# Kernel tuning notes

Hardware: AMD Instinct MI355X
Metric: run time of the kernel (lower is better)

Reference implementation:

```python
import jax, jax.numpy as jnp
import numpy as np

NUM_HEADS = 12
DIM = 768
HEAD_DIM = DIM // NUM_HEADS
NUM_BUCKETS = 32
MAX_DISTANCE = 128
ELEV_SCALE = 1000.0


def _bucket_positions(relative_position):
    # Faithful port of RelativePositionBias2D._bucket_positions (torch .long() truncates;
    # values passed through the large branch are non-negative so astype(int32) matches).
    nb = NUM_BUCKETS // 2  # 16
    n = -relative_position
    ret = (n < 0).astype(jnp.int32) * nb
    n = jnp.abs(n)
    max_exact = nb // 2  # 8
    is_small = n < max_exact
    n_safe = jnp.maximum(n, 1).astype(jnp.float32)  # avoid log(0); masked by is_small
    val_if_large = max_exact + (
        jnp.log(n_safe / max_exact) / np.float32(np.log(MAX_DISTANCE / max_exact)) * (nb - max_exact)
    ).astype(jnp.int32)
    val_if_large = jnp.minimum(val_if_large, nb - 1)
    return ret + jnp.where(is_small, n, val_if_large)


def _bucket_idx(coords_2d):
    # coords_2d: [B, N, 2] in [0,1] -> integer grid coords
    coords_int = (coords_2d * MAX_DISTANCE).astype(jnp.int32)
    rel_x = coords_int[:, :, None, 0] - coords_int[:, None, :, 0]  # [B,N,N]
    rel_y = coords_int[:, :, None, 1] - coords_int[:, None, :, 1]
    bx = _bucket_positions(rel_x)
    by = _bucket_positions(rel_y)
    return bx * NUM_BUCKETS + by  # [B,N,N] int32 in [0, 1024)


def setup_inputs() -> dict:
    key = jax.random.key(0)
    ks = jax.random.split(key, 8)
    B, N, D = 4, 1024, DIM
    x = jax.random.normal(ks[0], (B, N, D), dtype=jnp.float32)
    coords_2d = jax.random.uniform(ks[1], (B, N, 2), dtype=jnp.float32)
    elevation_patches = jax.random.normal(ks[2], (B, N), dtype=jnp.float32) * 2000.0  # meters
    qkv_w = jax.random.normal(ks[3], (3 * D, D), dtype=jnp.float32) * 0.02
    qkv_b = jnp.zeros((3 * D,), dtype=jnp.float32)
    proj_w = jax.random.normal(ks[4], (D, D), dtype=jnp.float32) * 0.02
    proj_b = jnp.zeros((D,), dtype=jnp.float32)
    bias_table = jax.random.normal(ks[5], (NUM_BUCKETS * NUM_BUCKETS, NUM_HEADS), dtype=jnp.float32) * 0.02
    alpha = jnp.full((1,), 2.0, dtype=jnp.float32)
    return {"x": x, "coords_2d": coords_2d, "elevation_patches": elevation_patches,
            "qkv_w": qkv_w, "qkv_b": qkv_b, "proj_w": proj_w, "proj_b": proj_b,
            "bias_table": bias_table, "alpha": alpha}


def reference(x, coords_2d, elevation_patches, qkv_w, qkv_b, proj_w, proj_b, bias_table, alpha):
    B, N, D = x.shape
    H, hd = NUM_HEADS, HEAD_DIM
    scale = hd ** -0.5

    qkv = x @ qkv_w.T + qkv_b  # [B,N,3D]
    qkv = qkv.reshape(B, N, 3, H, hd)
    q = qkv[:, :, 0].transpose(0, 2, 1, 3)  # [B,H,N,hd]
    k = qkv[:, :, 1].transpose(0, 2, 1, 3)
    v = qkv[:, :, 2].transpose(0, 2, 1, 3)

    attn = jnp.einsum('bhnd,bhmd->bhnm', q * scale, k)  # [B,H,N,N]

    # relative position bias: gather from table, [B,N,N,H] -> [B,H,N,N]
    idx = _bucket_idx(coords_2d)
    rel_bias = bias_table[idx].transpose(0, 3, 1, 2)
    attn = attn + rel_bias

    # elevation bias: [B,N,N], broadcast over heads
    elev_diff = (elevation_patches[:, None, :] - elevation_patches[:, :, None]) / ELEV_SCALE
    elev_bias = jnp.clip(-alpha[0] * jax.nn.relu(elev_diff), -10.0, 0.0)
    attn = attn + elev_bias[:, None, :, :]

    attn = jax.nn.softmax(attn.astype(jnp.float32), axis=-1).astype(q.dtype)

    out = jnp.einsum('bhnm,bhmd->bhnd', attn, v)  # [B,H,N,hd]
    out = out.transpose(0, 2, 1, 3).reshape(B, N, D)
    return out @ proj_w.T + proj_b
```

## Files before the change

kernel.cpp:

```cpp
#include <hip/hip_runtime.h>
#include <hip/hip_bf16.h>
#include <math.h>

#define NH 12
#define HD 64
#define NSEQ 1024
#define DMODEL 768
#define LOG2E 1.44269504f

typedef unsigned short ushort_t;
typedef float f32x4 __attribute__((ext_vector_type(4)));
typedef short bf16x8 __attribute__((ext_vector_type(8)));

__device__ __forceinline__ ushort_t f2bf(float f) {
    unsigned int u = __float_as_uint(f);
    u += 0x7FFFu + ((u >> 16) & 1u);
    return (ushort_t)(u >> 16);
}

__device__ __forceinline__ unsigned pk2(float x, float y) {
    __hip_bfloat162 t = __float22bfloat162_rn(make_float2(x, y));
    union { __hip_bfloat162 b; unsigned u; } c; c.b = t;
    return c.u;
}

__device__ __forceinline__ void gl_lds16(const ushort_t* g, ushort_t* l) {
    __builtin_amdgcn_global_load_lds(
        (const __attribute__((address_space(1))) unsigned int*)g,
        (__attribute__((address_space(3))) unsigned int*)l, 16, 0, 0);
}

#define XB_N   3145728u
#define WQB_N  1769472u
#define PWB_N  589824u
#define CVT_BLOCKS 2688

__device__ __forceinline__ int bucketf(int rel) {
    const int n = -rel;
    const int u = (n < 0) ? 16 : 0;
    const int a = n < 0 ? -n : n;
    if (a < 8) return u + a;
    int v = 8 + (int)(log2f((float)a * 0.125f) * 2.0f + 1e-4f);
    if (v > 15) v = 15;
    return u + v;
}

__global__ __launch_bounds__(256) void prep_kernel(
    const float* __restrict__ x, const float* __restrict__ w1,
    const float* __restrict__ w2, ushort_t* __restrict__ dst,
    const float* __restrict__ coords, const float* __restrict__ elev,
    const float* __restrict__ alpha_p, unsigned* __restrict__ pack)
{
    const int t = threadIdx.x;
    if (blockIdx.x < CVT_BLOCKS) {
        const unsigned i = blockIdx.x * 256 + t;
        const unsigned n0 = XB_N / 8, n1 = n0 + WQB_N / 8, n2 = n1 + PWB_N / 8;
        if (i >= n2) return;
        const float* src; unsigned off;
        if (i < n0)      { src = x;  off = i; }
        else if (i < n1) { src = w1; off = i - n0; }
        else             { src = w2; off = i - n1; }
        const float4 a = ((const float4*)src)[off * 2];
        const float4 b = ((const float4*)src)[off * 2 + 1];
        uint4 pk;
        pk.x = pk2(a.x, a.y); pk.y = pk2(a.z, a.w);
        pk.z = pk2(b.x, b.y); pk.w = pk2(b.z, b.w);
        ((uint4*)dst)[i] = pk;
    } else {
        const int blk = blockIdx.x - CVT_BLOCKS;
        const int b = blk >> 10, i = blk & 1023;
        const float alpha = alpha_p[0];
        const float2 ci = *(const float2*)&coords[(size_t)(b * NSEQ + i) * 2];
        const int cxi = (int)(ci.x * 128.0f), cyi = (int)(ci.y * 128.0f);
        const float ei = elev[b * NSEQ + i];
        const int j0 = t * 4;
        const float4 c01 = *(const float4*)&coords[(size_t)(b * NSEQ + j0) * 2];
        const float4 c23 = *(const float4*)&coords[(size_t)(b * NSEQ + j0 + 2) * 2];
        const float4 ej4 = *(const float4*)&elev[b * NSEQ + j0];
        const float cjx[4] = {c01.x, c01.z, c23.x, c23.z};
        const float cjy[4] = {c01.y, c01.w, c23.y, c23.w};
        const float ejv[4] = {ej4.x, ej4.y, ej4.z, ej4.w};
        unsigned r[4];
        #pragma unroll
        for (int k = 0; k < 4; ++k) {
            const int bx = bucketf(cxi - (int)(cjx[k] * 128.0f));
            const int by = bucketf(cyi - (int)(cjy[k] * 128.0f));
            const int idx = (bx << 5) + by;
            const float ed = (ejv[k] - ei) * 1e-3f;
            const float eb = fmaxf(-alpha * fmaxf(ed, 0.0f), -10.0f) * LOG2E;
            r[k] = ((unsigned)f2bf(eb) << 16) | (unsigned)idx;
        }
        uint4 o; o.x = r[0]; o.y = r[1]; o.z = r[2]; o.w = r[3];
        *(uint4*)&pack[((size_t)b << 20) + (size_t)i * NSEQ + j0] = o;
    }
}

__global__ __launch_bounds__(256) void qkv_gemm(
    const ushort_t* __restrict__ A, const ushort_t* __restrict__ B,
    const float* __restrict__ bias,
    ushort_t* __restrict__ Qb, ushort_t* __restrict__ Kb, ushort_t* __restrict__ Vtb)
{
    __shared__ __align__(16) ushort_t SM[6144];
    ushort_t* Asb = SM;
    ushort_t* Bsb = SM + 4096;
    const int t = threadIdx.x;
    const int lane = t & 63, w = t >> 6;
    const int wr = w >> 1, wc = w & 1;
    const int col = lane & 15, quad = lane >> 4;
    const int m0 = blockIdx.y * 128, c0 = blockIdx.x * 64;

    const f32x4 zero = {0.f, 0.f, 0.f, 0.f};
    f32x4 acc[4][2];
    #pragma unroll
    for (int i = 0; i < 4; ++i)
        #pragma unroll
        for (int j = 0; j < 2; ++j) acc[i][j] = zero;

    const int arow = w * 32 + (lane >> 2);
    const int brow = w * 16 + (lane >> 2);
    const int scol = (lane & 3) * 8;
    const ushort_t* Ag = A + (size_t)(m0 + arow) * DMODEL + scol;
    const ushort_t* Bg = B + (size_t)(c0 + brow) * DMODEL + scol;
    ushort_t* Asw = Asb + w * 32 * 32;
    ushort_t* Bsw = Bsb + w * 16 * 32;

    for (int k0 = 0; k0 < DMODEL; k0 += 32) {
        __syncthreads();
        gl_lds16(Ag + k0, Asw);
        gl_lds16(Ag + (size_t)16 * DMODEL + k0, Asw + 16 * 32);
        gl_lds16(Bg + k0, Bsw);
        __syncthreads();
        bf16x8 af[4], bf[2];
        #pragma unroll
        for (int im = 0; im < 4; ++im)
            af[im] = *(const bf16x8*)&Asb[(wr * 64 + im * 16 + col) * 32 + quad * 8];
        #pragma unroll
        for (int jn = 0; jn < 2; ++jn)
            bf[jn] = *(const bf16x8*)&Bsb[(wc * 32 + jn * 16 + col) * 32 + quad * 8];
        #pragma unroll
        for (int im = 0; im < 4; ++im)
            #pragma unroll
            for (int jn = 0; jn < 2; ++jn)
                acc[im][jn] = __builtin_amdgcn_mfma_f32_16x16x32_bf16(af[im], bf[jn], acc[im][jn], 0, 0, 0);
    }

    const int s = c0 / DMODEL;
    const int h = (c0 % DMODEL) >> 6;
    const int b = m0 >> 10;
    const int bh = b * NH + h;
    const int n0 = (m0 & (NSEQ - 1)) + wr * 64;
    const int d0 = (c0 & 63);
    const int cb = c0 + wc * 32;

    __syncthreads();

    if (s < 2) {
        ushort_t* lt = SM + w * 1280;
        ushort_t* dst = (s == 0) ? Qb : Kb;
        const float sc = (s == 0) ? 0.125f * LOG2E : 1.0f;
        float bv[2];
        #pragma unroll
        for (int jn = 0; jn < 2; ++jn) bv[jn] = bias[cb + jn * 16 + col];
        const int row16 = lane >> 2, seg = lane & 3;
        #pragma unroll
        for (int im = 0; im < 4; ++im) {
            #pragma unroll
            for (int jn = 0; jn < 2; ++jn) {
                const f32x4 a = acc[im][jn];
                #pragma unroll
                for (int r = 0; r < 4; ++r)
                    lt[(quad * 4 + r) * 40 + jn * 16 + col] = f2bf((a[r] + bv[jn]) * sc);
            }
            const uint4 u0 = *(const uint4*)&lt[row16 * 40 + seg * 8];
            const size_t gb = ((size_t)bh * NSEQ + n0 + im * 16 + row16) * HD
                            + wc * 32 + seg * 8;
            *(uint4*)&dst[gb] = u0;
        }
    } else {
        #pragma unroll
        for (int im = 0; im < 4; ++im) {
            #pragma unroll
            for (int jn = 0; jn < 2; ++jn) {
                const int d = wc * 32 + jn * 16 + col;
                const float bvv = bias[cb + jn * 16 + col];
                const f32x4 a = acc[im][jn];
                uint2 p;
                p.x = pk2(a[0] + bvv, a[1] + bvv);
                p.y = pk2(a[2] + bvv, a[3] + bvv);
                *(uint2*)&Vtb[((size_t)bh * HD + d) * NSEQ + n0 + im * 16 + quad * 4] = p;
            }
        }
    }
    (void)d0;
}

#define RBIAS(u) (__uint_as_float((unsigned)tabu[(u) & 1023u] << 16) \
                + __uint_as_float((u) & 0xFFFF0000u))

__global__ __launch_bounds__(256) void attn_mfma(
    const ushort_t* __restrict__ Qb, const ushort_t* __restrict__ Kb,
    const ushort_t* __restrict__ Vtb,
    const unsigned* __restrict__ pack,
    const float* __restrict__ table,
    ushort_t* __restrict__ Ob)
{
    __shared__ __align__(16) ushort_t Ks[2][64 * 72];
    __shared__ __align__(16) ushort_t Vt[2][64 * 72];
    __shared__ __align__(16) ushort_t Ps[64 * 72];
    __shared__ ushort_t tabu[1024];

    const int t = threadIdx.x;
    const int lane = t & 63, w = t >> 6;
    const int col = lane & 15, quad = lane >> 4;
    const int bid = (blockIdx.x & 7) * 96 + (blockIdx.x >> 3);
    const int it = bid & 15, bh = bid >> 4;
    const int h = bh % NH, b = bh / NH;
    const int i0 = it * 64;

    for (int i = t; i < 1024; i += 256)
        tabu[i] = f2bf(table[i * NH + h] * LOG2E);

    const ushort_t* Qg = Qb + ((size_t)bh * NSEQ + i0 + w * 16 + col) * HD;
    const bf16x8 aq0 = *(const bf16x8*)(Qg + quad * 8);
    const bf16x8 aq1 = *(const bf16x8*)(Qg + 32 + quad * 8);

    const size_t kvbase = (size_t)bh * NSEQ * HD;
    const unsigned* prow = pack + ((size_t)b << 20)
                         + (size_t)(i0 + w * 16 + col) * NSEQ + quad * 4;

    const int srow = t >> 3, sc8 = (t & 7) * 8;
    const int so0 = srow * 72 + sc8;
    const int so1 = (srow + 32) * 72 + sc8;

    uint4 k0 = *(const uint4*)&Kb[kvbase + (size_t)srow * HD + sc8];
    uint4 k1 = *(const uint4*)&Kb[kvbase + (size_t)(srow + 32) * HD + sc8];
    uint4 v0 = *(const uint4*)&Vtb[kvbase + (size_t)srow * NSEQ + sc8];
    uint4 v1 = *(const uint4*)&Vtb[kvbase + (size_t)(srow + 32) * NSEQ + sc8];
    *(uint4*)&Ks[0][so0] = k0;
    *(uint4*)&Ks[0][so1] = k1;
    *(uint4*)&Vt[0][so0] = v0;
    *(uint4*)&Vt[0][so1] = v1;
    k0 = *(const uint4*)&Kb[kvbase + (size_t)(64 + srow) * HD + sc8];
    k1 = *(const uint4*)&Kb[kvbase + (size_t)(64 + srow + 32) * HD + sc8];
    v0 = *(const uint4*)&Vtb[kvbase + (size_t)srow * NSEQ + 64 + sc8];
    v1 = *(const uint4*)&Vtb[kvbase + (size_t)(srow + 32) * NSEQ + 64 + sc8];

    uint4 pk4g[4], pk4l[4];
    #pragma unroll
    for (int jb = 0; jb < 4; ++jb)
        pk4g[jb] = *(const uint4*)(prow + jb * 16);

    __syncthreads();

    float rbc[4][4], rbn[4][4];
    #pragma unroll
    for (int jb = 0; jb < 4; ++jb) {
        const uint4 pkv = pk4g[jb];
        rbc[jb][0] = RBIAS(pkv.x);
        rbc[jb][1] = RBIAS(pkv.y);
        rbc[jb][2] = RBIAS(pkv.z);
        rbc[jb][3] = RBIAS(pkv.w);
    }
    #pragma unroll
    for (int jb = 0; jb < 4; ++jb)
        pk4g[jb] = *(const uint4*)(prow + 64 + jb * 16);

    const f32x4 zero = {0.f, 0.f, 0.f, 0.f};
    f32x4 o_acc[4];
    #pragma unroll
    for (int i = 0; i < 4; ++i) o_acc[i] = zero;
    float l_l = 0.f;

    #pragma unroll 2
    for (int jt = 0; jt < 16; ++jt) {
        __syncthreads();
        const int cur = jt & 1;

        if (jt < 15) {
            *(uint4*)&Ks[cur ^ 1][so0] = k0;
            *(uint4*)&Ks[cur ^ 1][so1] = k1;
            *(uint4*)&Vt[cur ^ 1][so0] = v0;
            *(uint4*)&Vt[cur ^ 1][so1] = v1;
        }
        if (jt < 14) {
            const int j2 = (jt + 2) * 64;
            k0 = *(const uint4*)&Kb[kvbase + (size_t)(j2 + srow) * HD + sc8];
            k1 = *(const uint4*)&Kb[kvbase + (size_t)(j2 + srow + 32) * HD + sc8];
            v0 = *(const uint4*)&Vtb[kvbase + (size_t)srow * NSEQ + j2 + sc8];
            v1 = *(const uint4*)&Vtb[kvbase + (size_t)(srow + 32) * NSEQ + j2 + sc8];
            #pragma unroll
            for (int jb = 0; jb < 4; ++jb)
                pk4l[jb] = *(const uint4*)(prow + j2 + jb * 16);
        }

        f32x4 sacc[4];
        __builtin_amdgcn_s_setprio(1);
        #pragma unroll
        for (int jb = 0; jb < 4; ++jb) {
            sacc[jb] = zero;
            const bf16x8 kb0 = *(const bf16x8*)&Ks[cur][(jb * 16 + col) * 72 + quad * 8];
            const bf16x8 kb1 = *(const bf16x8*)&Ks[cur][(jb * 16 + col) * 72 + 32 + quad * 8];
            sacc[jb] = __builtin_amdgcn_mfma_f32_16x16x32_bf16(kb0, aq0, sacc[jb], 0, 0, 0);
            sacc[jb] = __builtin_amdgcn_mfma_f32_16x16x32_bf16(kb1, aq1, sacc[jb], 0, 0, 0);
        }
        __builtin_amdgcn_s_setprio(0);

        float psum = 0.f;
        #pragma unroll
        for (int jb = 0; jb < 4; ++jb) {
            const float p0 = exp2f(sacc[jb][0] + rbc[jb][0]);
            const float p1 = exp2f(sacc[jb][1] + rbc[jb][1]);
            const float p2 = exp2f(sacc[jb][2] + rbc[jb][2]);
            const float p3 = exp2f(sacc[jb][3] + rbc[jb][3]);
            psum += (p0 + p1) + (p2 + p3);
            uint2 st;
            st.x = pk2(p0, p1);
            st.y = pk2(p2, p3);
            *(uint2*)&Ps[(w * 16 + col) * 72 + jb * 16 + quad * 4] = st;
        }
        l_l += psum;

        const bf16x8 ap0 = *(const bf16x8*)&Ps[(w * 16 + col) * 72 + quad * 8];
        const bf16x8 ap1 = *(const bf16x8*)&Ps[(w * 16 + col) * 72 + 32 + quad * 8];
        __builtin_amdgcn_s_setprio(1);
        #pragma unroll
        for (int db = 0; db < 4; ++db) {
            const bf16x8 vv0 = *(const bf16x8*)&Vt[cur][(db * 16 + col) * 72 + quad * 8];
            const bf16x8 vv1 = *(const bf16x8*)&Vt[cur][(db * 16 + col) * 72 + 32 + quad * 8];
            o_acc[db] = __builtin_amdgcn_mfma_f32_16x16x32_bf16(ap0, vv0, o_acc[db], 0, 0, 0);
            o_acc[db] = __builtin_amdgcn_mfma_f32_16x16x32_bf16(ap1, vv1, o_acc[db], 0, 0, 0);
            if (jt < 15) {
                const uint4 pkv = pk4g[db];
                rbn[db][0] = RBIAS(pkv.x);
                rbn[db][1] = RBIAS(pkv.y);
                rbn[db][2] = RBIAS(pkv.z);
                rbn[db][3] = RBIAS(pkv.w);
            }
        }
        __builtin_amdgcn_s_setprio(0);

        #pragma unroll
        for (int jb = 0; jb < 4; ++jb) {
            pk4g[jb] = pk4l[jb];
            rbc[jb][0] = rbn[jb][0];
            rbc[jb][1] = rbn[jb][1];
            rbc[jb][2] = rbn[jb][2];
            rbc[jb][3] = rbn[jb][3];
        }
    }

    float l = l_l;
    l += __shfl_xor(l, 16);
    l += __shfl_xor(l, 32);
    #pragma unroll
    for (int r = 0; r < 4; ++r) {
        const float lr = __shfl(l, w * 16 + quad * 4 + r);
        const float inv = 1.f / lr;
        const int ri = w * 16 + quad * 4 + r;
        const size_t base = ((size_t)(b * NSEQ) + i0 + ri) * DMODEL + h * HD;
        #pragma unroll
        for (int db = 0; db < 4; ++db)
            Ob[base + db * 16 + col] = f2bf(o_acc[db][r] * inv);
    }
}

__global__ __launch_bounds__(256) void proj_gemm(
    const ushort_t* __restrict__ A, const ushort_t* __restrict__ B,
    const float* __restrict__ bias, float* __restrict__ out)
{
    __shared__ __align__(16) ushort_t As[64 * 32];
    __shared__ __align__(16) ushort_t Bs[64 * 32];
    const int t = threadIdx.x;
    const int lane = t & 63, w = t >> 6;
    const int wr = w >> 1, wc = w & 1;
    const int col = lane & 15, quad = lane >> 4;
    const int m0 = blockIdx.y * 64, c0 = blockIdx.x * 64;

    const f32x4 zero = {0.f, 0.f, 0.f, 0.f};
    f32x4 acc[2][2];
    #pragma unroll
    for (int i = 0; i < 2; ++i)
        #pragma unroll
        for (int j = 0; j < 2; ++j) acc[i][j] = zero;

    const int srow = w * 16 + (lane >> 2);
    const int scol = (lane & 3) * 8;
    const ushort_t* Ag = A + (size_t)(m0 + srow) * DMODEL + scol;
    const ushort_t* Bg = B + (size_t)(c0 + srow) * DMODEL + scol;
    ushort_t* Asw = &As[w * 16 * 32];
    ushort_t* Bsw = &Bs[w * 16 * 32];

    for (int k0 = 0; k0 < DMODEL; k0 += 32) {
        __syncthreads();
        gl_lds16(Ag + k0, Asw);
        gl_lds16(Bg + k0, Bsw);
        __syncthreads();
        bf16x8 af[2], bf[2];
        #pragma unroll
        for (int im = 0; im < 2; ++im)
            af[im] = *(const bf16x8*)&As[(wr * 32 + im * 16 + col) * 32 + quad * 8];
        #pragma unroll
        for (int jn = 0; jn < 2; ++jn)
            bf[jn] = *(const bf16x8*)&Bs[(wc * 32 + jn * 16 + col) * 32 + quad * 8];
        #pragma unroll
        for (int im = 0; im < 2; ++im)
            #pragma unroll
            for (int jn = 0; jn < 2; ++jn)
                acc[im][jn] = __builtin_amdgcn_mfma_f32_16x16x32_bf16(af[im], bf[jn], acc[im][jn], 0, 0, 0);
    }

    #pragma unroll
    for (int im = 0; im < 2; ++im) {
        #pragma unroll
        for (int jn = 0; jn < 2; ++jn) {
            const int c = c0 + wc * 32 + jn * 16 + col;
            const float bv = bias[c];
            #pragma unroll
            for (int r = 0; r < 4; ++r) {
                const int m = m0 + wr * 32 + im * 16 + quad * 4 + r;
                out[(size_t)m * DMODEL + c] = acc[im][jn][r] + bv;
            }
        }
    }
}

extern "C" void kernel_launch(void* const* d_in, const int* in_sizes, int n_in,
                              void* d_out, int out_size, void* d_ws, size_t ws_size,
                              hipStream_t stream) {
    const float* x       = (const float*)d_in[0];
    const float* coords  = (const float*)d_in[1];
    const float* elev    = (const float*)d_in[2];
    const float* qkv_w   = (const float*)d_in[3];
    const float* qkv_b   = (const float*)d_in[4];
    const float* proj_w  = (const float*)d_in[5];
    const float* proj_b  = (const float*)d_in[6];
    const float* btable  = (const float*)d_in[7];
    const float* alpha   = (const float*)d_in[8];
    float* out = (float*)d_out;

    ushort_t* wsu = (ushort_t*)d_ws;
    ushort_t* xb  = wsu;
    ushort_t* wqb = wsu + 3145728;
    ushort_t* pwb = wsu + 4915200;
    ushort_t* Qb  = wsu + 5505024;
    ushort_t* Kb  = wsu + 8650752;
    ushort_t* Vtb = wsu + 11796480;
    ushort_t* Ob  = wsu + 14942208;
    unsigned* pck = (unsigned*)(wsu + 18087936);

    prep_kernel<<<CVT_BLOCKS + 4096, 256, 0, stream>>>(
        x, qkv_w, proj_w, wsu, coords, elev, alpha, pck);
    qkv_gemm<<<dim3(36, 32), 256, 0, stream>>>(xb, wqb, qkv_b, Qb, Kb, Vtb);
    attn_mfma<<<768, 256, 0, stream>>>(Qb, Kb, Vtb, pck, btable, Ob);
    proj_gemm<<<dim3(12, 64), 256, 0, stream>>>(Ob, pwb, proj_b, out);
}
```

Baseline: 185.9 us.

## Widen QKV GEMM tiles to 128x128, remap blocks, and fuse bias-pack prep into it

The QKV GEMM output tile grows from 128x64 to 128x128, so each warp computes a 64x64 sub-tile with 16 MFMA accumulators and each A/B tile load is reused more. Block indices are remapped through a 1D grid swizzle, intended to improve L2 locality. The position/elevation pack computation moves out of the conversion kernel and into extra blocks of the QKV GEMM launch, so it can overlap with GEMM work. The cost is higher register pressure and fewer GEMM blocks (576), which could reduce occupancy or leave compute units unevenly loaded.

Result: no change. 182.7 us (-1.7%).

```diff
diff --git a/kernel.cpp b/kernel.cpp
--- a/kernel.cpp
+++ b/kernel.cpp
@@ -34,6 +34,26 @@
 #define WQB_N  1769472u
 #define PWB_N  589824u
 #define CVT_BLOCKS 2688
+
+__global__ __launch_bounds__(256) void prep_kernel(
+    const float* __restrict__ x, const float* __restrict__ w1,
+    const float* __restrict__ w2, ushort_t* __restrict__ dst)
+{
+    const int t = threadIdx.x;
+    const unsigned i = blockIdx.x * 256 + t;
+    const unsigned n0 = XB_N / 8, n1 = n0 + WQB_N / 8, n2 = n1 + PWB_N / 8;
+    if (i >= n2) return;
+    const float* src; unsigned off;
+    if (i < n0)      { src = x;  off = i; }
+    else if (i < n1) { src = w1; off = i - n0; }
+    else             { src = w2; off = i - n1; }
+    const float4 a = ((const float4*)src)[off * 2];
+    const float4 b = ((const float4*)src)[off * 2 + 1];
+    uint4 pk;
+    pk.x = pk2(a.x, a.y); pk.y = pk2(a.z, a.w);
+    pk.z = pk2(b.x, b.y); pk.w = pk2(b.z, b.w);
+    ((uint4*)dst)[i] = pk;
+}
 
 __device__ __forceinline__ int bucketf(int rel) {
     const int n = -rel;
@@ -45,29 +65,20 @@
     return u + v;
 }
 
-__global__ __launch_bounds__(256) void prep_kernel(
-    const float* __restrict__ x, const float* __restrict__ w1,
-    const float* __restrict__ w2, ushort_t* __restrict__ dst,
+#define QKV_BLOCKS 576
+
+__global__ __launch_bounds__(256) void qkv_gemm(
+    const ushort_t* __restrict__ A, const ushort_t* __restrict__ B,
+    const float* __restrict__ bias,
+    ushort_t* __restrict__ Qb, ushort_t* __restrict__ Kb, ushort_t* __restrict__ Vtb,
     const float* __restrict__ coords, const float* __restrict__ elev,
     const float* __restrict__ alpha_p, unsigned* __restrict__ pack)
 {
+    __shared__ __align__(16) ushort_t SM[9216];
     const int t = threadIdx.x;
-    if (blockIdx.x < CVT_BLOCKS) {
-        const unsigned i = blockIdx.x * 256 + t;
-        const unsigned n0 = XB_N / 8, n1 = n0 + WQB_N / 8, n2 = n1 + PWB_N / 8;
-        if (i >= n2) return;
-        const float* src; unsigned off;
-        if (i < n0)      { src = x;  off = i; }
-        else if (i < n1) { src = w1; off = i - n0; }
-        else             { src = w2; off = i - n1; }
-        const float4 a = ((const float4*)src)[off * 2];
-        const float4 b = ((const float4*)src)[off * 2 + 1];
-        uint4 pk;
-        pk.x = pk2(a.x, a.y); pk.y = pk2(a.z, a.w);
-        pk.z = pk2(b.x, b.y); pk.w = pk2(b.z, b.w);
-        ((uint4*)dst)[i] = pk;
-    } else {
-        const int blk = blockIdx.x - CVT_BLOCKS;
+
+    if (blockIdx.x >= QKV_BLOCKS) {
+        const int blk = blockIdx.x - QKV_BLOCKS;
         const int b = blk >> 10, i = blk & 1023;
         const float alpha = alpha_p[0];
         const float2 ci = *(const float2*)&coords[(size_t)(b * NSEQ + i) * 2];
@@ -92,97 +103,95 @@
         }
         uint4 o; o.x = r[0]; o.y = r[1]; o.z = r[2]; o.w = r[3];
         *(uint4*)&pack[((size_t)b << 20) + (size_t)i * NSEQ + j0] = o;
-    }
-}
-
-__global__ __launch_bounds__(256) void qkv_gemm(
-    const ushort_t* __restrict__ A, const ushort_t* __restrict__ B,
-    const float* __restrict__ bias,
-    ushort_t* __restrict__ Qb, ushort_t* __restrict__ Kb, ushort_t* __restrict__ Vtb)
-{
-    __shared__ __align__(16) ushort_t SM[6144];
+        return;
+    }
+
+    const int lid = (blockIdx.x & 7) * 72 + (blockIdx.x >> 3);
+    const int bx = lid % 18, by = lid / 18;
+    const int m0 = by * 128, c0 = bx * 128;
+
     ushort_t* Asb = SM;
     ushort_t* Bsb = SM + 4096;
-    const int t = threadIdx.x;
     const int lane = t & 63, w = t >> 6;
     const int wr = w >> 1, wc = w & 1;
     const int col = lane & 15, quad = lane >> 4;
-    const int m0 = blockIdx.y * 128, c0 = blockIdx.x * 64;
 
     const f32x4 zero = {0.f, 0.f, 0.f, 0.f};
-    f32x4 acc[4][2];
+    f32x4 acc[4][4];
     #pragma unroll
     for (int i = 0; i < 4; ++i)
         #pragma unroll
-        for (int j = 0; j < 2; ++j) acc[i][j] = zero;
+        for (int j = 0; j < 4; ++j) acc[i][j] = zero;
 
     const int arow = w * 32 + (lane >> 2);
-    const int brow = w * 16 + (lane >> 2);
     const int scol = (lane & 3) * 8;
     const ushort_t* Ag = A + (size_t)(m0 + arow) * DMODEL + scol;
-    const ushort_t* Bg = B + (size_t)(c0 + brow) * DMODEL + scol;
+    const ushort_t* Bg = B + (size_t)(c0 + arow) * DMODEL + scol;
     ushort_t* Asw = Asb + w * 32 * 32;
-    ushort_t* Bsw = Bsb + w * 16 * 32;
+    ushort_t* Bsw = Bsb + w * 32 * 32;
 
     for (int k0 = 0; k0 < DMODEL; k0 += 32) {
         __syncthreads();
         gl_lds16(Ag + k0, Asw);
         gl_lds16(Ag + (size_t)16 * DMODEL + k0, Asw + 16 * 32);
         gl_lds16(Bg + k0, Bsw);
+        gl_lds16(Bg + (size_t)16 * DMODEL + k0, Bsw + 16 * 32);
         __syncthreads();
-        bf16x8 af[4], bf[2];
+        bf16x8 af[4], bf[4];
         #pragma unroll
         for (int im = 0; im < 4; ++im)
             af[im] = *(const bf16x8*)&Asb[(wr * 64 + im * 16 + col) * 32 + quad * 8];
         #pragma unroll
-        for (int jn = 0; jn < 2; ++jn)
-            bf[jn] = *(const bf16x8*)&Bsb[(wc * 32 + jn * 16 + col) * 32 + quad * 8];
+        for (int jn = 0; jn < 4; ++jn)
+            bf[jn] = *(const bf16x8*)&Bsb[(wc * 64 + jn * 16 + col) * 32 + quad * 8];
         #pragma unroll
         for (int im = 0; im < 4; ++im)
             #pragma unroll
-            for (int jn = 0; jn < 2; ++jn)
+            for (int jn = 0; jn < 4; ++jn)
                 acc[im][jn] = __builtin_amdgcn_mfma_f32_16x16x32_bf16(af[im], bf[jn], acc[im][jn], 0, 0, 0);
     }
 
-    const int s = c0 / DMODEL;
-    const int h = (c0 % DMODEL) >> 6;
+    const int cbw = c0 + wc * 64;
+    const int s = cbw / DMODEL;
+    const int h = (cbw % DMODEL) >> 6;
     const int b = m0 >> 10;
     const int bh = b * NH + h;
     const int n0 = (m0 & (NSEQ - 1)) + wr * 64;
-    const int d0 = (c0 & 63);
-    const int cb = c0 + wc * 32;
+
+    float bv[4];
+    #pragma unroll
+    for (int jn = 0; jn < 4; ++jn) bv[jn] = bias[cbw + jn * 16 + col];
 
     __syncthreads();
 
     if (s < 2) {
-        ushort_t* lt = SM + w * 1280;
+        ushort_t* lt = SM + w * 1152;
         ushort_t* dst = (s == 0) ? Qb : Kb;
         const float sc = (s == 0) ? 0.125f * LOG2E : 1.0f;
-        float bv[2];
-        #pragma unroll
-        for (int jn = 0; jn < 2; ++jn) bv[jn] = bias[cb + jn * 16 + col];
         const int row16 = lane >> 2, seg = lane & 3;
         #pragma unroll
         for (int im = 0; im < 4; ++im) {
             #pragma unroll
-            for (int jn = 0; jn < 2; ++jn) {
+            for (int jn = 0; jn < 4; ++jn) {
                 const f32x4 a = acc[im][jn];
                 #pragma unroll
                 for (int r = 0; r < 4; ++r)
-                    lt[(quad * 4 + r) * 40 + jn * 16 + col] = f2bf((a[r] + bv[jn]) * sc);
+                    lt[(quad * 4 + r) * 72 + jn * 16 + col] = f2bf((a[r] + bv[jn]) * sc);
             }
-            const uint4 u0 = *(const uint4*)&lt[row16 * 40 + seg * 8];
+            const uint4 u0 = *(const uint4*)&lt[row16 * 72 + seg * 8];
+            const uint4 u1 = *(const uint4*)&lt[row16 * 72 + 32 + seg * 8];
             const size_t gb = ((size_t)bh * NSEQ + n0 + im * 16 + row16) * HD
-                            + wc * 32 + seg * 8;
+                            + seg * 8;
             *(uint4*)&dst[gb] = u0;
+            *(uint4*)&dst[gb + 32] = u1;
         }
     } else {
         #pragma unroll
         for (int im = 0; im < 4; ++im) {
             #pragma unroll
-            for (int jn = 0; jn < 2; ++jn) {
-                const int d = wc * 32 + jn * 16 + col;
-                const float bvv = bias[cb + jn * 16 + col];
+            for (int jn = 0; jn < 4; ++jn) {
+                const int d = jn * 16 + col;
+                const float bvv = bv[jn];
                 const f32x4 a = acc[im][jn];
                 uint2 p;
                 p.x = pk2(a[0] + bvv, a[1] + bvv);
@@ -191,7 +200,6 @@
             }
         }
     }
-    (void)d0;
 }
 
 #define RBIAS(u) (__uint_as_float((unsigned)tabu[(u) & 1023u] << 16) \
@@ -448,9 +456,9 @@
     ushort_t* Ob  = wsu + 14942208;
     unsigned* pck = (unsigned*)(wsu + 18087936);
 
-    prep_kernel<<<CVT_BLOCKS + 4096, 256, 0, stream>>>(
-        x, qkv_w, proj_w, wsu, coords, elev, alpha, pck);
-    qkv_gemm<<<dim3(36, 32), 256, 0, stream>>>(xb, wqb, qkv_b, Qb, Kb, Vtb);
+    prep_kernel<<<CVT_BLOCKS, 256, 0, stream>>>(x, qkv_w, proj_w, wsu);
+    qkv_gemm<<<QKV_BLOCKS + 4096, 256, 0, stream>>>(
+        xb, wqb, qkv_b, Qb, Kb, Vtb, coords, elev, alpha, pck);
     attn_mfma<<<768, 256, 0, stream>>>(Qb, Kb, Vtb, pck, btable, Ob);
     proj_gemm<<<dim3(12, 64), 256, 0, stream>>>(Ob, pwb, proj_b, out);
 }
```
